# Optimization experiments

Measured on AMD Instinct MI355X. Metric: run time of the kernel, lower is better.

The kernel has to match this reference:

```python
import jax, jax.numpy as jnp
from jax import lax
import numpy as np

B, T, R, U = 32, 32, 256, 4  # batch, exposures, recon size, upscale (2**(lambda_scale_factor-1))
YS = R // U                  # yt_img_size = 64


def setup_inputs() -> dict:
    key = jax.random.key(0)
    k = jax.random.split(key, 6)
    yt = jax.random.normal(k[0], (B, T, YS, YS), dtype=jnp.float32)
    Ht = jax.random.normal(k[1], (T, R, R), dtype=jnp.float32) * 0.1
    W1 = jax.random.normal(k[2], (32, 1, 3, 3), dtype=jnp.float32) * 0.1
    b1 = jnp.zeros((32,), dtype=jnp.float32)
    W2 = jax.random.normal(k[3], (1, 32, 3, 3), dtype=jnp.float32) * 0.1
    b2 = jnp.zeros((1,), dtype=jnp.float32)
    return {"yt": yt, "Ht": Ht, "W1": W1, "b1": b1, "W2": W2, "b2": b2}


def _conv(x, w, b):
    # NCHW / OIHW, stride 1, SAME padding
    y = lax.conv_general_dilated(x, w, window_strides=(1, 1), padding="SAME",
                                 dimension_numbers=("NCHW", "OIHW", "NCHW"))
    return y + b[None, :, None, None]


def reference(yt, Ht, W1, b1, W2, b2):
    # Structured A^T @ yt without materializing the (R^2, T*YS^2) sparse matrix:
    # out[b,p,q] = sum_t Ht[t,p,q] * yt[b,t,p//U,q//U]
    yt_up = jnp.repeat(jnp.repeat(yt, U, axis=2), U, axis=3)      # (B,T,R,R) nearest upsample
    x = jnp.einsum("btpq,tpq->bpq", yt_up, Ht)[:, None]            # (B,1,R,R)
    # upsample_postproc_block: Conv(1->32,3x3) -> ReLU -> Conv(32->1,3x3)
    x = jax.nn.relu(_conv(x, W1, b1))
    x = _conv(x, W2, b2)
    return x
```

## Files before the change

kernel.cpp:

```cpp
#include <hip/hip_runtime.h>

#define R 256
#define T 32

#define TROWS 8
#define TCOLS 32
#define HR 10
#define HC 34
#define HSTR 36
#define CP 360
#define WSLICE (4 * CP)
#define NPX (HR * HC)
#define NPAIR (NPX / 2)

typedef float v2f __attribute__((ext_vector_type(2)));
#define FMA2(a, b, c) __builtin_elementwise_fma((a), (b), (c))

__global__ __launch_bounds__(256) void einsum_kernel(
    const float* __restrict__ yt, const float* __restrict__ Ht,
    float* __restrict__ x) {
  const int idx = blockIdx.x;
  const int rh  = idx >> 8;
  const int yy  = (idx & 255) >> 2;
  const int bq  = idx & 3;
  const int b0  = bq * 8;
  const int tid = threadIdx.x;
  const int q   = tid;
  const int q4  = q >> 2;

  __shared__ float yts[8 * 32 * 64];

#pragma unroll
  for (int i = 0; i < 16; ++i) {
    int f4  = tid + i * 256;
    int b_l = f4 >> 9;
    int t   = (f4 >> 4) & 31;
    int xx4 = f4 & 15;
    float4 v = *(const float4*)(yt + (((size_t)(b0 + b_l) * T + t) * 64 + yy) * 64 + xx4 * 4);
    *(float4*)(yts + f4 * 4) = v;
  }
  __syncthreads();

  for (int rr = 0; rr < 2; ++rr) {
    const int p = yy * 4 + rh * 2 + rr;
    float ht[T];
#pragma unroll
    for (int t = 0; t < T; ++t) ht[t] = Ht[((size_t)t * R + p) * R + q];

#pragma unroll
    for (int b_l = 0; b_l < 8; ++b_l) {
      const float* ys = yts + b_l * 2048 + q4;
      float acc = 0.f;
#pragma unroll
      for (int t = 0; t < T; ++t) acc += ht[t] * ys[t * 64];
      x[((size_t)(b0 + b_l) * R + p) * R + q] = acc;
    }
  }
}

template <bool EDGE>
__device__ __forceinline__ void conv_body(
    const v2f (&patch2)[3][9], bool slot2, const bool (&oob)[6],
    const int (&sw)[3], float* hs,
    const float* __restrict__ W1, const float* __restrict__ b1,
    const float* __restrict__ W2, int cl, int hboff, v2f (&acc2)[4][2]) {
  for (int cg = 0; cg < 8; ++cg) {
    float w2[9];
#pragma unroll
    for (int k = 0; k < 9; ++k) w2[k] = W2[(cg * 4 + cl) * 9 + k];

#pragma unroll
    for (int c = 0; c < 4; ++c) {
      const int ch = cg * 4 + c;
      const float bias = b1[ch];
      v2f h0 = {bias, bias}, h1 = {bias, bias}, h2 = {bias, bias};
#pragma unroll
      for (int k = 0; k < 9; ++k) {
        const float w = W1[ch * 9 + k];
        const v2f wv = {w, w};
        h0 = FMA2(wv, patch2[0][k], h0);
        h1 = FMA2(wv, patch2[1][k], h1);
        h2 = FMA2(wv, patch2[2][k], h2);
      }
      const v2f z = {0.f, 0.f};
      h0 = __builtin_elementwise_max(h0, z);
      h1 = __builtin_elementwise_max(h1, z);
      h2 = __builtin_elementwise_max(h2, z);
      if (EDGE) {
        if (oob[0]) h0.x = 0.f;
        if (oob[1]) h0.y = 0.f;
        if (oob[2]) h1.x = 0.f;
        if (oob[3]) h1.y = 0.f;
        if (oob[4]) h2.x = 0.f;
        if (oob[5]) h2.y = 0.f;
      }
      float* hp = hs + c * CP;
      *(v2f*)(hp + sw[0]) = h0;
      *(v2f*)(hp + sw[1]) = h1;
      if (slot2) *(v2f*)(hp + sw[2]) = h2;
    }

#pragma unroll
    for (int j = 0; j < 6; ++j) {
      float4 v4 = *(const float4*)(hs + hboff + j * HSTR);
      float2 vt = *(const float2*)(hs + hboff + j * HSTR + 4);
      v2f P[5];
      P[0] = (v2f){v4.x, v4.y};
      P[1] = (v2f){v4.y, v4.z};
      P[2] = (v2f){v4.z, v4.w};
      P[3] = (v2f){v4.w, vt.x};
      P[4] = (v2f){vt.x, vt.y};
#pragma unroll
      for (int dy = 0; dy < 3; ++dy) {
        int ai = j - dy;
        if (ai >= 0 && ai < 4) {
#pragma unroll
          for (int dx = 0; dx < 3; ++dx) {
            const float w = w2[dy * 3 + dx];
            const v2f wv = {w, w};
            acc2[ai][0] = FMA2(wv, P[dx], acc2[ai][0]);
            acc2[ai][1] = FMA2(wv, P[dx + 2], acc2[ai][1]);
          }
        }
      }
    }
  }
}

template <bool EDGE>
__device__ __forceinline__ void conv_tile(
    const float* __restrict__ xb, int ty0, int ox0, int lane, float* hsw,
    const float* __restrict__ W1, const float* __restrict__ b1,
    const float* __restrict__ W2, const float* __restrict__ b2,
    float* __restrict__ outp) {
  v2f  patch2[3][9];
  int  sw[3];
  bool oob[6];
  const bool slot2 = (lane < NPAIR - 2 * 64);
#pragma unroll
  for (int it = 0; it < 3; ++it) {
    int pi = lane + it * 64;
    bool act = (it < 2) || slot2;
    int px0 = 2 * pi;
    int hy  = act ? (px0 / HC) : 0;
    int hx0 = act ? (px0 % HC) : 0;
    sw[it] = hy * HSTR + hx0;
    int ghy = ty0 - 1 + hy;
    int ghx0 = ox0 - 1 + hx0;
    bool rowok = (ghy >= 0) & (ghy < R);
    oob[2 * it]     = !(rowok & (ghx0 >= 0) & (ghx0 < R));
    oob[2 * it + 1] = !(rowok & (ghx0 + 1 >= 0) & (ghx0 + 1 < R));
#pragma unroll
    for (int ky = 0; ky < 3; ++ky) {
      const int gy  = ty0 - 2 + hy + ky;
      const int gx0 = ox0 - 2 + hx0;
      v2f fa, fb;
      if (EDGE) {
        float xv[4];
#pragma unroll
        for (int c = 0; c < 4; ++c) {
          int gx = gx0 + c;
          bool ok = act & (gy >= 0) & (gy < R) & (gx >= 0) & (gx < R);
          xv[c] = ok ? xb[gy * R + gx] : 0.f;
        }
        fa = (v2f){xv[0], xv[1]};
        fb = (v2f){xv[2], xv[3]};
      } else {
        const float* xp = xb + gy * R + gx0;
        fa = act ? *(const v2f*)(xp)     : (v2f){0.f, 0.f};
        fb = act ? *(const v2f*)(xp + 2) : (v2f){0.f, 0.f};
      }
      patch2[it][3 * ky + 0] = fa;
      patch2[it][3 * ky + 1] = (v2f){fa.y, fb.x};
      patch2[it][3 * ky + 2] = fb;
    }
  }

  const int g  = lane & 7;
  const int cl = (lane >> 3) & 3;
  const int rh = lane >> 5;
  const int r0 = 4 * rh;

  v2f acc2[4][2];
#pragma unroll
  for (int ai = 0; ai < 4; ++ai) {
    acc2[ai][0] = (v2f){0.f, 0.f};
    acc2[ai][1] = (v2f){0.f, 0.f};
  }

  const int hboff = cl * CP + r0 * HSTR + 4 * g;

  conv_body<EDGE>(patch2, slot2, oob, sw, hsw, W1, b1, W2, cl, hboff, acc2);

  const float bias2 = b2[0];
#pragma unroll
  for (int ai = 0; ai < 4; ++ai)
#pragma unroll
    for (int h = 0; h < 2; ++h) {
      float vx = acc2[ai][h].x, vy = acc2[ai][h].y;
      vx += __shfl_xor(vx, 8);  vy += __shfl_xor(vy, 8);
      vx += __shfl_xor(vx, 16); vy += __shfl_xor(vy, 16);
      acc2[ai][h].x = vx; acc2[ai][h].y = vy;
    }
  if (cl == 0) {
#pragma unroll
    for (int ai = 0; ai < 4; ++ai) {
      float4 o = {acc2[ai][0].x + bias2, acc2[ai][0].y + bias2,
                  acc2[ai][1].x + bias2, acc2[ai][1].y + bias2};
      *(float4*)(outp + (ty0 + r0 + ai) * R + ox0 + 4 * g) = o;
    }
  }
}

__global__ __launch_bounds__(256) void conv_fused_kernel(
    const float* __restrict__ x, const float* __restrict__ W1,
    const float* __restrict__ b1, const float* __restrict__ W2,
    const float* __restrict__ b2, float* __restrict__ out) {
  __shared__ float hs[4 * WSLICE];

  const int tid  = threadIdx.x;
  const int lane = tid & 63;
  const int wv   = tid >> 6;
  const int b    = blockIdx.x >> 6;
  const int tile = blockIdx.x & 63;
  const int ty0  = (tile >> 3) * 32 + wv * TROWS;
  const int ox0  = (tile & 7) * TCOLS;
  const float* xb   = x + (size_t)b * R * R;
  float*       outp = out + (size_t)b * R * R;
  float*       hsw  = hs + wv * WSLICE;

  const bool edge = (ty0 == 0) | (ty0 == R - TROWS) | (ox0 == 0) | (ox0 == R - TCOLS);
  if (edge)
    conv_tile<true>(xb, ty0, ox0, lane, hsw, W1, b1, W2, b2, outp);
  else
    conv_tile<false>(xb, ty0, ox0, lane, hsw, W1, b1, W2, b2, outp);
}

extern "C" void kernel_launch(void* const* d_in, const int* in_sizes, int n_in,
                              void* d_out, int out_size, void* d_ws, size_t ws_size,
                              hipStream_t stream) {
  const float* yt = (const float*)d_in[0];
  const float* Ht = (const float*)d_in[1];
  const float* W1 = (const float*)d_in[2];
  const float* b1 = (const float*)d_in[3];
  const float* W2 = (const float*)d_in[4];
  const float* b2 = (const float*)d_in[5];
  float* outp = (float*)d_out;
  float* x    = (float*)d_ws;

  einsum_kernel<<<512, 256, 0, stream>>>(yt, Ht, x);
  conv_fused_kernel<<<2048, 256, 0, stream>>>(x, W1, b1, W2, b2, outp);
}
```

Before: 130.6 us.

## Fuse einsum into conv kernel, computing x tile with halo in shared memory

Removes the separate einsum kernel and the intermediate x buffer in global memory. Each conv block now loads a 10x10 yt patch per exposure into LDS and computes its 36x36 x tile (with a 2-pixel halo) directly from Ht before running the fused conv. This saves one launch and the x write/read round trip. In exchange, Ht loads are repeated across all 32 batches and the halos are recomputed, and the LDS used for yt is shared with the hidden-activation buffer.

```diff
diff --git a/kernel.cpp b/kernel.cpp
--- a/kernel.cpp
+++ b/kernel.cpp
@@ -4,58 +4,21 @@
 #define T 32
 
 #define TROWS 8
-#define TCOLS 32
 #define HR 10
 #define HC 34
 #define HSTR 36
 #define CP 360
 #define WSLICE (4 * CP)
-#define NPX (HR * HC)
-#define NPAIR (NPX / 2)
+#define NPAIR 170
+
+#define XSN 1296
+#define YTN 3200
 
 typedef float v2f __attribute__((ext_vector_type(2)));
 #define FMA2(a, b, c) __builtin_elementwise_fma((a), (b), (c))
 
-__global__ __launch_bounds__(256) void einsum_kernel(
-    const float* __restrict__ yt, const float* __restrict__ Ht,
-    float* __restrict__ x) {
-  const int idx = blockIdx.x;
-  const int rh  = idx >> 8;
-  const int yy  = (idx & 255) >> 2;
-  const int bq  = idx & 3;
-  const int b0  = bq * 8;
-  const int tid = threadIdx.x;
-  const int q   = tid;
-  const int q4  = q >> 2;
-
-  __shared__ float yts[8 * 32 * 64];
-
-#pragma unroll
-  for (int i = 0; i < 16; ++i) {
-    int f4  = tid + i * 256;
-    int b_l = f4 >> 9;
-    int t   = (f4 >> 4) & 31;
-    int xx4 = f4 & 15;
-    float4 v = *(const float4*)(yt + (((size_t)(b0 + b_l) * T + t) * 64 + yy) * 64 + xx4 * 4);
-    *(float4*)(yts + f4 * 4) = v;
-  }
-  __syncthreads();
-
-  for (int rr = 0; rr < 2; ++rr) {
-    const int p = yy * 4 + rh * 2 + rr;
-    float ht[T];
-#pragma unroll
-    for (int t = 0; t < T; ++t) ht[t] = Ht[((size_t)t * R + p) * R + q];
-
-#pragma unroll
-    for (int b_l = 0; b_l < 8; ++b_l) {
-      const float* ys = yts + b_l * 2048 + q4;
-      float acc = 0.f;
-#pragma unroll
-      for (int t = 0; t < T; ++t) acc += ht[t] * ys[t * 64];
-      x[((size_t)(b0 + b_l) * R + p) * R + q] = acc;
-    }
-  }
+__device__ __forceinline__ int iclamp(int v, int lo, int hi) {
+  return min(max(v, lo), hi);
 }
 
 template <bool EDGE>
@@ -127,12 +90,69 @@
   }
 }
 
-template <bool EDGE>
-__device__ __forceinline__ void conv_tile(
-    const float* __restrict__ xb, int ty0, int ox0, int lane, float* hsw,
+__global__ __launch_bounds__(256) void fused_kernel(
+    const float* __restrict__ yt, const float* __restrict__ Ht,
     const float* __restrict__ W1, const float* __restrict__ b1,
     const float* __restrict__ W2, const float* __restrict__ b2,
-    float* __restrict__ outp) {
+    float* __restrict__ out) {
+  __shared__ float smem[XSN + 4 * WSLICE];
+  float* xs  = smem;
+  float* yts = smem + XSN;
+  float* hs  = smem + XSN;
+
+  const int tid  = threadIdx.x;
+  const int lane = tid & 63;
+  const int wv   = tid >> 6;
+  const int b    = blockIdx.x >> 6;
+  const int tile = blockIdx.x & 63;
+  const int oy0  = (tile >> 3) * 32;
+  const int ox0  = (tile & 7) * 32;
+  const int ty0  = oy0 + wv * TROWS;
+
+  const int ybase = oy0 / 4 - 1;
+  const int xbase = ox0 / 4 - 1;
+  for (int j = tid; j < YTN; j += 256) {
+    int t   = j / 100;
+    int rem = j - t * 100;
+    int yr  = rem / 10;
+    int yc  = rem - yr * 10;
+    int gy  = iclamp(ybase + yr, 0, 63);
+    int gx  = iclamp(xbase + yc, 0, 63);
+    yts[j] = yt[(((size_t)b * T + t) * 64 + gy) * 64 + gx];
+  }
+  __syncthreads();
+
+#pragma unroll
+  for (int s = 0; s < 3; ++s) {
+    int pi = tid + s * 256;
+    if (pi < 648) {
+      int px0 = 2 * pi;
+      int pr  = px0 / 36;
+      int pc  = px0 - pr * 36;
+      int p   = oy0 - 2 + pr;
+      int q0  = ox0 - 2 + pc;
+      int p_c = iclamp(p, 0, 255);
+      int q_c = iclamp(q0, 0, 254);
+      int yrl = (p_c >> 2) - ybase;
+      int ycl = (iclamp(q0, 0, 255) >> 2) - xbase;
+      const float* hp = Ht + (size_t)p_c * 256 + q_c;
+      const float* yp = yts + yrl * 10 + ycl;
+      v2f acc = {0.f, 0.f};
+#pragma unroll
+      for (int t = 0; t < T; ++t) {
+        v2f h2 = *(const v2f*)(hp + (size_t)t * 65536);
+        float yv = yp[t * 100];
+        v2f yv2 = {yv, yv};
+        acc = FMA2(h2, yv2, acc);
+      }
+      bool rok = (p >= 0) & (p < R);
+      if (!(rok & (q0 >= 0) & (q0 < R)))         acc.x = 0.f;
+      if (!(rok & (q0 + 1 >= 0) & (q0 + 1 < R))) acc.y = 0.f;
+      *(v2f*)(xs + pr * 36 + pc) = acc;
+    }
+  }
+  __syncthreads();
+
   v2f  patch2[3][9];
   int  sw[3];
   bool oob[6];
@@ -143,33 +163,18 @@
     bool act = (it < 2) || slot2;
     int px0 = 2 * pi;
     int hy  = act ? (px0 / HC) : 0;
-    int hx0 = act ? (px0 % HC) : 0;
+    int hx0 = act ? (px0 - (px0 / HC) * HC) : 0;
     sw[it] = hy * HSTR + hx0;
-    int ghy = ty0 - 1 + hy;
+    int ghy  = ty0 - 1 + hy;
     int ghx0 = ox0 - 1 + hx0;
     bool rowok = (ghy >= 0) & (ghy < R);
     oob[2 * it]     = !(rowok & (ghx0 >= 0) & (ghx0 < R));
-    oob[2 * it + 1] = !(rowok & (ghx0 + 1 >= 0) & (ghx0 + 1 < R));
+    oob[2 * it + 1] = !(rowok & (ghx0 + 1 < R));
 #pragma unroll
     for (int ky = 0; ky < 3; ++ky) {
-      const int gy  = ty0 - 2 + hy + ky;
-      const int gx0 = ox0 - 2 + hx0;
-      v2f fa, fb;
-      if (EDGE) {
-        float xv[4];
-#pragma unroll
-        for (int c = 0; c < 4; ++c) {
-          int gx = gx0 + c;
-          bool ok = act & (gy >= 0) & (gy < R) & (gx >= 0) & (gx < R);
-          xv[c] = ok ? xb[gy * R + gx] : 0.f;
-        }
-        fa = (v2f){xv[0], xv[1]};
-        fb = (v2f){xv[2], xv[3]};
-      } else {
-        const float* xp = xb + gy * R + gx0;
-        fa = act ? *(const v2f*)(xp)     : (v2f){0.f, 0.f};
-        fb = act ? *(const v2f*)(xp + 2) : (v2f){0.f, 0.f};
-      }
+      int base = (wv * TROWS + hy + ky) * 36 + hx0;
+      v2f fa = *(const v2f*)(xs + base);
+      v2f fb = *(const v2f*)(xs + base + 2);
       patch2[it][3 * ky + 0] = fa;
       patch2[it][3 * ky + 1] = (v2f){fa.y, fb.x};
       patch2[it][3 * ky + 2] = fb;
@@ -188,9 +193,14 @@
     acc2[ai][1] = (v2f){0.f, 0.f};
   }
 
+  float* hsw = hs + wv * WSLICE;
   const int hboff = cl * CP + r0 * HSTR + 4 * g;
 
-  conv_body<EDGE>(patch2, slot2, oob, sw, hsw, W1, b1, W2, cl, hboff, acc2);
+  const bool edge = (ty0 == 0) | (ty0 == R - TROWS) | (ox0 == 0) | (ox0 == R - 32);
+  if (edge)
+    conv_body<true>(patch2, slot2, oob, sw, hsw, W1, b1, W2, cl, hboff, acc2);
+  else
+    conv_body<false>(patch2, slot2, oob, sw, hsw, W1, b1, W2, cl, hboff, acc2);
 
   const float bias2 = b2[0];
 #pragma unroll
@@ -203,6 +213,7 @@
       acc2[ai][h].x = vx; acc2[ai][h].y = vy;
     }
   if (cl == 0) {
+    float* outp = out + (size_t)b * R * R;
 #pragma unroll
     for (int ai = 0; ai < 4; ++ai) {
       float4 o = {acc2[ai][0].x + bias2, acc2[ai][0].y + bias2,
@@ -210,30 +221,6 @@
       *(float4*)(outp + (ty0 + r0 + ai) * R + ox0 + 4 * g) = o;
     }
   }
-}
-
-__global__ __launch_bounds__(256) void conv_fused_kernel(
-    const float* __restrict__ x, const float* __restrict__ W1,
-    const float* __restrict__ b1, const float* __restrict__ W2,
-    const float* __restrict__ b2, float* __restrict__ out) {
-  __shared__ float hs[4 * WSLICE];
-
-  const int tid  = threadIdx.x;
-  const int lane = tid & 63;
-  const int wv   = tid >> 6;
-  const int b    = blockIdx.x >> 6;
-  const int tile = blockIdx.x & 63;
-  const int ty0  = (tile >> 3) * 32 + wv * TROWS;
-  const int ox0  = (tile & 7) * TCOLS;
-  const float* xb   = x + (size_t)b * R * R;
-  float*       outp = out + (size_t)b * R * R;
-  float*       hsw  = hs + wv * WSLICE;
-
-  const bool edge = (ty0 == 0) | (ty0 == R - TROWS) | (ox0 == 0) | (ox0 == R - TCOLS);
-  if (edge)
-    conv_tile<true>(xb, ty0, ox0, lane, hsw, W1, b1, W2, b2, outp);
-  else
-    conv_tile<false>(xb, ty0, ox0, lane, hsw, W1, b1, W2, b2, outp);
 }
 
 extern "C" void kernel_launch(void* const* d_in, const int* in_sizes, int n_in,
@@ -246,8 +233,6 @@
   const float* W2 = (const float*)d_in[4];
   const float* b2 = (const float*)d_in[5];
   float* outp = (float*)d_out;
-  float* x    = (float*)d_ws;
-
-  einsum_kernel<<<512, 256, 0, stream>>>(yt, Ht, x);
-  conv_fused_kernel<<<2048, 256, 0, stream>>>(x, W1, b1, W2, b2, outp);
-}
+
+  fused_kernel<<<2048, 256, 0, stream>>>(yt, Ht, W1, b1, W2, b2, outp);
+}
```

Result: slower. 145.4 us (+11.3%).
